# Kernel tuning notes

Hardware: AMD Instinct MI355X
Metric: run time of the kernel (lower is better)

Reference implementation:

```python
import jax, jax.numpy as jnp
import numpy as np

D_MODEL = 1024
N_HEADS = 16
D_HEAD = 64
SEQ = 2048
BATCH = 2
ATTN_SCALE = float(np.sqrt(D_HEAD))  # cfg.use_attn_scale = True
NEG_INF = -1e9


def setup_inputs() -> dict:
    key = jax.random.key(0)
    ks = jax.random.split(key, 8)
    s = 0.02
    return {
        "query_input": jax.random.normal(ks[0], (BATCH, SEQ, D_MODEL), jnp.float32),
        "key_input": jax.random.normal(ks[1], (BATCH, SEQ, D_MODEL), jnp.float32),
        "value_input": jax.random.normal(ks[2], (BATCH, SEQ, D_MODEL), jnp.float32),
        "W_Q": jax.random.normal(ks[3], (N_HEADS, D_MODEL, D_HEAD), jnp.float32) * s,
        "W_K": jax.random.normal(ks[4], (N_HEADS, D_MODEL, D_HEAD), jnp.float32) * s,
        "W_V": jax.random.normal(ks[5], (N_HEADS, D_MODEL, D_HEAD), jnp.float32) * s,
        "W_O": jax.random.normal(ks[6], (N_HEADS, D_HEAD, D_MODEL), jnp.float32) * s,
        "b_Q": jnp.zeros((N_HEADS, D_HEAD), jnp.float32),
        "b_K": jnp.zeros((N_HEADS, D_HEAD), jnp.float32),
        "b_V": jnp.zeros((N_HEADS, D_HEAD), jnp.float32),
        "b_O": jnp.zeros((D_MODEL,), jnp.float32),
    }


def reference(query_input, key_input, value_input, W_Q, W_K, W_V, W_O, b_Q, b_K, b_V, b_O):
    # QKV projections: [batch, pos, d_model] x [head, d_model, d_head] -> [batch, pos, head, d_head]
    q = jnp.einsum("bpd,hde->bphe", query_input, W_Q) + b_Q
    k = jnp.einsum("bpd,hde->bphe", key_input, W_K) + b_K
    v = jnp.einsum("bpd,hde->bphe", value_input, W_V) + b_V

    # attn scores [batch, head, query_pos, key_pos]
    scores = jnp.einsum("bqhe,bkhe->bhqk", q, k) / ATTN_SCALE

    # causal mask (attn_type == 'global'): tril over [n_ctx, n_ctx] sliced to seq
    causal = jnp.tril(jnp.ones((SEQ, SEQ), bool))
    scores = jnp.where(causal[None, None, :, :], scores, NEG_INF)

    pattern = jax.nn.softmax(scores, axis=-1)

    # z: [batch, query_pos, head, d_head]
    z = jnp.einsum("bhqk,bkhe->bqhe", pattern, v)

    # output projection: [batch, pos, d_model]
    out = jnp.einsum("bqhe,hed->bqd", z, W_O) + b_O
    return out
```

## Files before the change

### kernel.cpp

```cpp
#include <hip/hip_runtime.h>
#include <stdint.h>


typedef __attribute__((ext_vector_type(8))) short short8;
typedef __attribute__((ext_vector_type(4))) short short4v;
typedef __attribute__((ext_vector_type(4))) float floatx4;
typedef __attribute__((ext_vector_type(4))) unsigned int uintx4;
typedef __attribute__((ext_vector_type(2))) unsigned int uint2v;

#define MFMA16(a, b, c) __builtin_amdgcn_mfma_f32_16x16x32_bf16(a, b, c, 0, 0, 0)

#if __has_builtin(__builtin_amdgcn_mfma_f32_16x16x16bf16_1k)
#define HAVE_K16 1
#define MFMAK16(a, b, c) __builtin_amdgcn_mfma_f32_16x16x16bf16_1k(a, b, c, 0, 0, 0)
#else
#define HAVE_K16 0
#endif

__device__ __forceinline__ unsigned short f2b(float f) {
  unsigned int u = __builtin_bit_cast(unsigned int, f);
  u = (u + 0x7fffu + ((u >> 16) & 1u)) >> 16;
  return (unsigned short)u;
}
__device__ __forceinline__ float exp2f_fast(float x) {
#if __has_builtin(__builtin_amdgcn_exp2f)
  return __builtin_amdgcn_exp2f(x);
#else
  return exp2f(x);
#endif
}
__device__ __forceinline__ unsigned int pack2_bf16(float lo, float hi) {
#if __has_builtin(__builtin_amdgcn_perm)
  return __builtin_amdgcn_perm(__builtin_bit_cast(unsigned int, hi),
                               __builtin_bit_cast(unsigned int, lo), 0x07060302u);
#else
  return (__builtin_bit_cast(unsigned int, lo) >> 16) |
         (__builtin_bit_cast(unsigned int, hi) & 0xffff0000u);
#endif
}

__device__ __forceinline__ void async_copy16(void* lds, const void* g) {
  __builtin_amdgcn_global_load_lds(
      (const __attribute__((address_space(1))) unsigned int*)g,
      (__attribute__((address_space(3))) unsigned int*)lds, 16, 0, 0);
}

__device__ __forceinline__ void xpose4(floatx4& v, int lane) {
  {
    float s0 = __shfl_xor(v[1], 1, 64);
    float s1 = __shfl_xor(v[0], 1, 64);
    float s2 = __shfl_xor(v[3], 1, 64);
    float s3 = __shfl_xor(v[2], 1, 64);
    if (lane & 1) { v[0] = s0; v[2] = s2; } else { v[1] = s1; v[3] = s3; }
  }
  {
    float s0 = __shfl_xor(v[2], 2, 64);
    float s1 = __shfl_xor(v[3], 2, 64);
    float s2 = __shfl_xor(v[0], 2, 64);
    float s3 = __shfl_xor(v[1], 2, 64);
    if (lane & 2) { v[0] = s0; v[1] = s1; } else { v[2] = s2; v[3] = s3; }
  }
}

__global__ __launch_bounds__(256) void convall(
    const float* __restrict__ Xq, const float* __restrict__ Xk,
    const float* __restrict__ Xv, const float* __restrict__ WQ,
    const float* __restrict__ WK, const float* __restrict__ WV,
    const float* __restrict__ WO, unsigned short* __restrict__ xout,
    unsigned short* __restrict__ wout, unsigned short* __restrict__ woout) {
  __shared__ float T[64][65];
  const int bid = blockIdx.x;
  const int t = threadIdx.x;
  if (bid < 12288) {
    const int yy = bid / 4096, x = bid - yy * 4096;
    const float* in = (yy == 0) ? Xq : ((yy == 1) ? Xk : Xv);
    size_t i = (size_t)x * 256 + t;
    float4 v = ((const float4*)in)[i];
    ushort4 u;
    u.x = f2b(v.x); u.y = f2b(v.y); u.z = f2b(v.z); u.w = f2b(v.w);
    ((ushort4*)(xout + (size_t)yy * 4194304))[i] = u;
    return;
  }
  const int rr = t >> 4, cc = t & 15;
  if (bid < 13056) {
    const int sub = bid - 12288;
    const int yy = sub >> 8, x = sub & 255;
    const float* in = (yy == 0) ? WQ : ((yy == 1) ? WK : WV);
    const int h = x >> 4, d0 = (x & 15) << 6;
#pragma unroll
    for (int it = 0; it < 4; ++it) {
      int dl = it * 16 + rr;
      float4 v = *(const float4*)&in[(size_t)h * 65536 + (size_t)(d0 + dl) * 64 + cc * 4];
      T[dl][cc * 4 + 0] = v.x; T[dl][cc * 4 + 1] = v.y;
      T[dl][cc * 4 + 2] = v.z; T[dl][cc * 4 + 3] = v.w;
    }
    __syncthreads();
    unsigned short* ob = wout + (size_t)yy * 1048576;
#pragma unroll
    for (int it = 0; it < 4; ++it) {
      int e = it * 16 + rr;
      ushort4 u;
      u.x = f2b(T[cc * 4 + 0][e]); u.y = f2b(T[cc * 4 + 1][e]);
      u.z = f2b(T[cc * 4 + 2][e]); u.w = f2b(T[cc * 4 + 3][e]);
      *(ushort4*)&ob[(size_t)(h * 64 + e) * 1024 + d0 + cc * 4] = u;
    }
    return;
  }
  {
    const int x = bid - 13056;
    const int r0 = (x & 15) << 6, c0 = (x >> 4) << 6;
#pragma unroll
    for (int it = 0; it < 4; ++it) {
      int rl = it * 16 + rr;
      float4 v = *(const float4*)&WO[(size_t)(r0 + rl) * 1024 + c0 + cc * 4];
      T[rl][cc * 4 + 0] = v.x; T[rl][cc * 4 + 1] = v.y;
      T[rl][cc * 4 + 2] = v.z; T[rl][cc * 4 + 3] = v.w;
    }
    __syncthreads();
#pragma unroll
    for (int it = 0; it < 4; ++it) {
      int dl = it * 16 + rr;
      ushort4 u;
      u.x = f2b(T[cc * 4 + 0][dl]); u.y = f2b(T[cc * 4 + 1][dl]);
      u.z = f2b(T[cc * 4 + 2][dl]); u.w = f2b(T[cc * 4 + 3][dl]);
      *(ushort4*)&woout[(size_t)(c0 + dl) * 1024 + r0 + cc * 4] = u;
    }
  }
}

template <int TM, int NZ>
__global__ __launch_bounds__(512, (TM == 128) ? 6 : 4) void gemm512(
    const short* __restrict__ A0, const short* __restrict__ A1,
    const short* __restrict__ A2, const short* __restrict__ B0,
    const short* __restrict__ B1, const short* __restrict__ B2,
    const float* __restrict__ bias0, const float* __restrict__ bias1,
    const float* __restrict__ bias2, unsigned short* __restrict__ ob0,
    unsigned short* __restrict__ ob1, unsigned short* __restrict__ ob2,
    float* __restrict__ outf, float qscale) {
  constexpr int WAVES_N = (TM == 128) ? 2 : 4;
  constexpr int NJ = (TM == 128) ? 4 : 2;
  constexpr int NY = 4096 / TM;
  __shared__ short As[TM * 64];
  __shared__ short Bs[128 * 64];

  const int L = blockIdx.x;
  const int x = L / (NY * NZ);
  const int r = L - x * (NY * NZ);
  const int y = r / NZ;
  const int z = r - y * NZ;

  const short* A = (z == 0) ? A0 : (z == 1) ? A1 : A2;
  const short* Bt = (z == 0) ? B0 : (z == 1) ? B1 : B2;

  const int tid = threadIdx.x;
  const int lane = tid & 63, w = tid >> 6;
  const int quad = lane >> 4, col = lane & 15;
  const int m0 = y * TM, n0 = x * 128;
  const int wm = (w / WAVES_N) * 32, wn = (w % WAVES_N) * (NJ * 16);

  floatx4 acc[2][NJ] = {};

  const int slr = lane >> 3, sgc = (lane & 7) ^ slr;
  const short* ga = A + (size_t)(m0 + w * (TM / 8) + slr) * 1024 + sgc * 8;
  const short* gb = Bt + (size_t)(n0 + w * 16 + slr) * 1024 + sgc * 8;
  const int fsw = col & 7;

  for (int k0 = 0; k0 < 1024; k0 += 64) {
    if (TM == 128) {
      async_copy16(&As[(w * 16) * 64], ga);
      async_copy16(&As[(w * 16 + 8) * 64], ga + 8 * 1024);
    } else {
      async_copy16(&As[(w * 8) * 64], ga);
    }
    async_copy16(&Bs[(w * 16) * 64], gb);
    async_copy16(&Bs[(w * 16 + 8) * 64], gb + 8 * 1024);
    ga += 64; gb += 64;
    __syncthreads();
#pragma unroll
    for (int kk = 0; kk < 2; ++kk) {
      short8 af[2], bf[NJ];
#pragma unroll
      for (int mi = 0; mi < 2; ++mi)
        af[mi] = *(const short8*)&As[(wm + mi * 16 + col) * 64 +
                                     (((kk * 4 + quad) ^ fsw) * 8)];
#pragma unroll
      for (int nj = 0; nj < NJ; ++nj)
        bf[nj] = *(const short8*)&Bs[(wn + nj * 16 + col) * 64 +
                                     (((kk * 4 + quad) ^ fsw) * 8)];
#pragma unroll
      for (int mi = 0; mi < 2; ++mi)
#pragma unroll
        for (int nj = 0; nj < NJ; ++nj)
          acc[mi][nj] = MFMA16(af[mi], bf[nj], acc[mi][nj]);
    }
    __syncthreads();
  }

  const float* bias = (z == 0) ? bias0 : (z == 1) ? bias1 : bias2;
  unsigned short* outb = (z == 0) ? ob0 : (z == 1) ? ob1 : ob2;
  const int mode = (NZ == 3) ? ((z == 2) ? 2 : 1) : 0;
  const float scale = (NZ == 3 && z == 0) ? qscale : 1.0f;

  float bv[NJ];
#pragma unroll
  for (int nj = 0; nj < NJ; ++nj) bv[nj] = bias[n0 + wn + nj * 16 + col];

  if (mode == 2) {
#pragma unroll
    for (int mi = 0; mi < 2; ++mi)
#pragma unroll
      for (int nj = 0; nj < NJ; ++nj) {
        int m = m0 + wm + mi * 16 + quad * 4;
        int n = n0 + wn + nj * 16 + col;
        int bb = m >> 11, s = m & 2047, h = n >> 6, e = n & 63;
        ushort4 u;
        u.x = f2b(acc[mi][nj][0] + bv[nj]);
        u.y = f2b(acc[mi][nj][1] + bv[nj]);
        u.z = f2b(acc[mi][nj][2] + bv[nj]);
        u.w = f2b(acc[mi][nj][3] + bv[nj]);
        *(ushort4*)&outb[(((size_t)bb * 16 + h) * 64 + e) * 2048 + s] = u;
      }
  } else {
#pragma unroll
    for (int mi = 0; mi < 2; ++mi)
#pragma unroll
      for (int nj = 0; nj < NJ; ++nj) {
        floatx4 v;
#pragma unroll
        for (int rr = 0; rr < 4; ++rr) v[rr] = (acc[mi][nj][rr] + bv[nj]) * scale;
        xpose4(v, lane);
        int m = m0 + wm + mi * 16 + quad * 4 + (col & 3);
        int nb = n0 + wn + nj * 16 + (col & ~3);
        if (mode == 0) {
          *(floatx4*)&outf[(size_t)m * 1024 + nb] = v;
        } else {
          int bb = m >> 11, s = m & 2047, h = nb >> 6, e = nb & 63;
          ushort4 u;
          u.x = f2b(v[0]); u.y = f2b(v[1]); u.z = f2b(v[2]); u.w = f2b(v[3]);
          *(ushort4*)&outb[(((size_t)bb * 16 + h) * 2048 + s) * 64 + e] = u;
        }
      }
  }
}

#if !HAVE_K16
__device__ __forceinline__ void exchange4(const unsigned int* u01,
                                          const unsigned int* u23, int srcA,
                                          int srcB, bool hiq, short8& pf0,
                                          short8& pf1) {
  unsigned int xA0 = (unsigned int)__shfl((int)u01[0], srcA, 64);
  unsigned int xA1 = (unsigned int)__shfl((int)u01[1], srcA, 64);
  unsigned int yA0 = (unsigned int)__shfl((int)u23[0], srcA, 64);
  unsigned int yA1 = (unsigned int)__shfl((int)u23[1], srcA, 64);
  unsigned int xB0 = (unsigned int)__shfl((int)u01[0], srcB, 64);
  unsigned int xB1 = (unsigned int)__shfl((int)u01[1], srcB, 64);
  unsigned int yB0 = (unsigned int)__shfl((int)u23[0], srcB, 64);
  unsigned int yB1 = (unsigned int)__shfl((int)u23[1], srcB, 64);
  uintx4 v0;
  v0.x = hiq ? xA1 : xA0; v0.y = hiq ? yA1 : yA0;
  v0.z = hiq ? xB1 : xB0; v0.w = hiq ? yB1 : yB0;
  pf0 = __builtin_bit_cast(short8, v0);
  xA0 = (unsigned int)__shfl((int)u01[2], srcA, 64);
  xA1 = (unsigned int)__shfl((int)u01[3], srcA, 64);
  yA0 = (unsigned int)__shfl((int)u23[2], srcA, 64);
  yA1 = (unsigned int)__shfl((int)u23[3], srcA, 64);
  xB0 = (unsigned int)__shfl((int)u01[2], srcB, 64);
  xB1 = (unsigned int)__shfl((int)u01[3], srcB, 64);
  yB0 = (unsigned int)__shfl((int)u23[2], srcB, 64);
  yB1 = (unsigned int)__shfl((int)u23[3], srcB, 64);
  uintx4 v1;
  v1.x = hiq ? xA1 : xA0; v1.y = hiq ? yA1 : yA0;
  v1.z = hiq ? xB1 : xB0; v1.w = hiq ? yB1 : yB0;
  pf1 = __builtin_bit_cast(short8, v1);
}
#endif

__device__ __forceinline__ void stage_kv(short* Kbuf, short* Vbuf,
                                         const short* kg, const short* vg,
                                         int kv0, int w, int slr, int sgc) {
  const short* kr = kg + (size_t)(kv0 + w * 16 + slr) * 64 + sgc * 8;
  async_copy16(&Kbuf[(w * 16) * 64], kr);
  async_copy16(&Kbuf[(w * 16 + 8) * 64], kr + 8 * 64);
  const short* vr = vg + (size_t)(w * 16 + slr) * 2048 + kv0 + sgc * 8;
  async_copy16(&Vbuf[(w * 16) * 64], vr);
  async_copy16(&Vbuf[(w * 16 + 8) * 64], vr + 8 * 2048);
}

__global__ __launch_bounds__(256) void attn(const short* __restrict__ q,
                                            const short* __restrict__ k,
                                            const short* __restrict__ vt,
                                            unsigned short* __restrict__ z) {
  __shared__ short Ks[2][64 * 64];
  __shared__ short Vs[2][64 * 64];

  const int tid = threadIdx.x;
  const int lane = tid & 63, w = tid >> 6;
  const int quad = lane >> 4, col = lane & 15;
  const int qt = 31 - (blockIdx.x >> 5), bh = blockIdx.x & 31;
  const int q0 = qt * 64, qw0 = q0 + w * 16;
  const size_t base = (size_t)bh * (2048 * 64);

  const short* qp = q + base + (size_t)(qw0 + col) * 64 + quad * 8;
  short8 bq0 = *(const short8*)qp;
  short8 bq1 = *(const short8*)(qp + 32);

  floatx4 o[4] = {};
  float m_run = -1e30f, l_run = 0.f;

  const short* kg = k + base;
  const short* vg = vt + base;
  const int ksw = col & 7;
  const int slr = lane >> 3, sgc = (lane & 7) ^ slr;
#if !HAVE_K16
  const int srcA = ((quad & 1) << 5) + col, srcB = srcA + 16;
  const bool hiq = (quad & 2) != 0;
#endif

  stage_kv(Ks[0], Vs[0], kg, vg, 0, w, slr, sgc);
  int p = 0;

  for (int t = 0; t <= qt; ++t) {
    __syncthreads();
    if (t < qt) stage_kv(Ks[p ^ 1], Vs[p ^ 1], kg, vg, (t + 1) * 64, w, slr, sgc);

    const bool diag = (t == qt);
    const int mtmax = diag ? w : 3;

    floatx4 st[4];
#pragma unroll
    for (int mt = 0; mt < 4; ++mt) {
      if (mt <= mtmax) {
        const short* kb = &Ks[p][(mt * 16 + col) * 64];
        short8 ka0 = *(const short8*)(kb + (quad ^ ksw) * 8);
        short8 ka1 = *(const short8*)(kb + ((quad + 4) ^ ksw) * 8);
        floatx4 a = {0.f, 0.f, 0.f, 0.f};
        a = MFMA16(ka0, bq0, a);
        a = MFMA16(ka1, bq1, a);
        if (diag && mt == mtmax) {
#pragma unroll
          for (int r = 0; r < 4; ++r)
            if (quad * 4 + r > col) a[r] = -1e9f;
        }
        st[mt] = a;
      }
    }

    float pmax = -3e38f;
#pragma unroll
    for (int mt = 0; mt < 4; ++mt)
      if (mt <= mtmax) {
#pragma unroll
        for (int r = 0; r < 4; ++r) pmax = fmaxf(pmax, st[mt][r]);
      }
    pmax = fmaxf(pmax, __shfl_xor(pmax, 16, 64));
    pmax = fmaxf(pmax, __shfl_xor(pmax, 32, 64));
    float mnew = fmaxf(m_run, pmax);
    float alpha = exp2f_fast(m_run - mnew);
    m_run = mnew;

    unsigned int u01[4], u23[4];
    float lsum = 0.f;
#pragma unroll
    for (int mt = 0; mt < 4; ++mt) {
      if (mt <= mtmax) {
        float p0 = exp2f_fast(st[mt][0] - mnew);
        float p1 = exp2f_fast(st[mt][1] - mnew);
        float p2 = exp2f_fast(st[mt][2] - mnew);
        float p3 = exp2f_fast(st[mt][3] - mnew);
        lsum += (p0 + p1) + (p2 + p3);
        u01[mt] = pack2_bf16(p0, p1);
        u23[mt] = pack2_bf16(p2, p3);
      } else {
        u01[mt] = 0u; u23[mt] = 0u;
      }
    }
    lsum += __shfl_xor(lsum, 16, 64);
    lsum += __shfl_xor(lsum, 32, 64);
    l_run = l_run * alpha + lsum;

#if HAVE_K16
    short4v pb[4];
#pragma unroll
    for (int mt = 0; mt < 4; ++mt) {
      uint2v uu;
      uu.x = u01[mt]; uu.y = u23[mt];
      pb[mt] = __builtin_bit_cast(short4v, uu);
    }
#pragma unroll
    for (int et = 0; et < 4; ++et) {
      const short* vrow = &Vs[p][(et * 16 + col) * 64];
      floatx4 t0 = o[et];
#pragma unroll
      for (int r = 0; r < 4; ++r) t0[r] *= alpha;
#pragma unroll
      for (int mt = 0; mt < 4; ++mt) {
        if (mt <= mtmax) {
          int c = mt * 2 + (quad >> 1);
          short4v va = *(const short4v*)&vrow[((c ^ ksw) * 8) + (quad & 1) * 4];
          t0 = MFMAK16(va, pb[mt], t0);
        }
      }
      o[et] = t0;
    }
#else
    short8 pf0, pf1;
    exchange4(u01, u23, srcA, srcB, hiq, pf0, pf1);
#pragma unroll
    for (int et = 0; et < 4; ++et) {
      const short* vb = &Vs[p][(et * 16 + col) * 64];
      short8 va0 = *(const short8*)(vb + (quad ^ ksw) * 8);
      short8 va1 = *(const short8*)(vb + ((quad + 4) ^ ksw) * 8);
      floatx4 t0 = o[et];
#pragma unroll
      for (int r = 0; r < 4; ++r) t0[r] *= alpha;
      t0 = MFMA16(va0, pf0, t0);
      t0 = MFMA16(va1, pf1, t0);
      o[et] = t0;
    }
#endif
    p ^= 1;
  }

  const int b = bh >> 4, h = bh & 15;
#if __has_builtin(__builtin_amdgcn_rcpf)
  const float invl = __builtin_amdgcn_rcpf(l_run);
#else
  const float invl = 1.f / l_run;
#endif
  unsigned short* zr = z + (((size_t)b * 2048 + qw0 + col) * 16 + h) * 64;
#pragma unroll
  for (int et = 0; et < 4; ++et) {
    ushort4 u;
    u.x = f2b(o[et][0] * invl); u.y = f2b(o[et][1] * invl);
    u.z = f2b(o[et][2] * invl); u.w = f2b(o[et][3] * invl);
    *(ushort4*)&zr[et * 16 + quad * 4] = u;
  }
}

extern "C" void kernel_launch(void* const* d_in, const int* in_sizes, int n_in,
                              void* d_out, int out_size, void* d_ws, size_t ws_size,
                              hipStream_t stream) {
  (void)in_sizes; (void)n_in; (void)out_size; (void)ws_size;
  const float* Xq = (const float*)d_in[0];
  const float* Xk = (const float*)d_in[1];
  const float* Xv = (const float*)d_in[2];
  const float* WQ = (const float*)d_in[3];
  const float* WK = (const float*)d_in[4];
  const float* WV = (const float*)d_in[5];
  const float* WO = (const float*)d_in[6];
  const float* bQ = (const float*)d_in[7];
  const float* bK = (const float*)d_in[8];
  const float* bV = (const float*)d_in[9];
  const float* bO = (const float*)d_in[10];
  float* out = (float*)d_out;

  unsigned short* xqb = (unsigned short*)d_ws;
  unsigned short* xkb = xqb + 4194304;
  unsigned short* xvb = xkb + 4194304;
  unsigned short* wqt = xvb + 4194304;
  unsigned short* wkt = wqt + 1048576;
  unsigned short* wvt = wkt + 1048576;
  unsigned short* wot = wvt + 1048576;
  unsigned short* qb = wot + 1048576;
  unsigned short* kb = qb + 4194304;
  unsigned short* vtb = kb + 4194304;
  unsigned short* zb = vtb + 4194304;

  convall<<<13312, 256, 0, stream>>>(Xq, Xk, Xv, WQ, WK, WV, WO, xqb, wqt, wot);

  const float qscale = 0.125f * 1.44269504088896f;
  gemm512<128, 3><<<768, 512, 0, stream>>>(
      (const short*)xqb, (const short*)xkb, (const short*)xvb,
      (const short*)wqt, (const short*)wkt, (const short*)wvt, bQ, bK, bV, qb,
      kb, vtb, nullptr, qscale);

  attn<<<1024, 256, 0, stream>>>((const short*)qb, (const short*)kb,
                                 (const short*)vtb, zb);

  gemm512<64, 1><<<512, 512, 0, stream>>>(
      (const short*)zb, (const short*)zb, (const short*)zb, (const short*)wot,
      (const short*)wot, (const short*)wot, bO, bO, bO, nullptr, nullptr,
      nullptr, out, 1.0f);
}
```

Measured before the change: 218.4 us.

## Split-K the output projection GEMM with atomic accumulation

Splits the K dimension of the output-projection GEMM into two halves, which doubles the block count from 512 to 1024 to fill the GPU better. Each half adds its partial sum into the float output with atomicAdd, and only the first half adds the bias. The output now has to be zeroed by a memset first. That adds an extra pass over 16 MB of memory plus scalar atomic traffic, and the launch bounds for the TM=64 variant change as well.

Result: slower. 312.3 us (+43.0%).

```diff
diff --git a/kernel.cpp b/kernel.cpp
--- a/kernel.cpp
+++ b/kernel.cpp
@@ -128,8 +128,8 @@
   }
 }
 
-template <int TM, int NZ>
-__global__ __launch_bounds__(512, (TM == 128) ? 6 : 4) void gemm512(
+template <int TM, int NZ, int KS>
+__global__ __launch_bounds__(512, 6) void gemm512(
     const short* __restrict__ A0, const short* __restrict__ A1,
     const short* __restrict__ A2, const short* __restrict__ B0,
     const short* __restrict__ B1, const short* __restrict__ B2,
@@ -144,10 +144,12 @@
   __shared__ short Bs[128 * 64];
 
   const int L = blockIdx.x;
-  const int x = L / (NY * NZ);
-  const int r = L - x * (NY * NZ);
-  const int y = r / NZ;
-  const int z = r - y * NZ;
+  const int x = L / (NY * NZ * KS);
+  const int r0d = L - x * (NY * NZ * KS);
+  const int y = r0d / (NZ * KS);
+  const int r1d = r0d - y * (NZ * KS);
+  const int z = r1d / KS;
+  const int ks = r1d - z * KS;
 
   const short* A = (z == 0) ? A0 : (z == 1) ? A1 : A2;
   const short* Bt = (z == 0) ? B0 : (z == 1) ? B1 : B2;
@@ -161,11 +163,12 @@
   floatx4 acc[2][NJ] = {};
 
   const int slr = lane >> 3, sgc = (lane & 7) ^ slr;
-  const short* ga = A + (size_t)(m0 + w * (TM / 8) + slr) * 1024 + sgc * 8;
-  const short* gb = Bt + (size_t)(n0 + w * 16 + slr) * 1024 + sgc * 8;
+  const int kbase = ks * (1024 / KS);
+  const short* ga = A + (size_t)(m0 + w * (TM / 8) + slr) * 1024 + kbase + sgc * 8;
+  const short* gb = Bt + (size_t)(n0 + w * 16 + slr) * 1024 + kbase + sgc * 8;
   const int fsw = col & 7;
 
-  for (int k0 = 0; k0 < 1024; k0 += 64) {
+  for (int k0 = 0; k0 < 1024 / KS; k0 += 64) {
     if (TM == 128) {
       async_copy16(&As[(w * 16) * 64], ga);
       async_copy16(&As[(w * 16 + 8) * 64], ga + 8 * 1024);
@@ -200,6 +203,7 @@
   unsigned short* outb = (z == 0) ? ob0 : (z == 1) ? ob1 : ob2;
   const int mode = (NZ == 3) ? ((z == 2) ? 2 : 1) : 0;
   const float scale = (NZ == 3 && z == 0) ? qscale : 1.0f;
+  const float bmul = (KS == 1 || ks == 0) ? 1.0f : 0.0f;
 
   float bv[NJ];
 #pragma unroll
@@ -227,12 +231,21 @@
       for (int nj = 0; nj < NJ; ++nj) {
         floatx4 v;
 #pragma unroll
-        for (int rr = 0; rr < 4; ++rr) v[rr] = (acc[mi][nj][rr] + bv[nj]) * scale;
+        for (int rr = 0; rr < 4; ++rr)
+          v[rr] = (acc[mi][nj][rr] + bv[nj] * bmul) * scale;
         xpose4(v, lane);
         int m = m0 + wm + mi * 16 + quad * 4 + (col & 3);
         int nb = n0 + wn + nj * 16 + (col & ~3);
         if (mode == 0) {
-          *(floatx4*)&outf[(size_t)m * 1024 + nb] = v;
+          float* op = &outf[(size_t)m * 1024 + nb];
+          if (KS == 2) {
+            atomicAdd(op + 0, v[0]);
+            atomicAdd(op + 1, v[1]);
+            atomicAdd(op + 2, v[2]);
+            atomicAdd(op + 3, v[3]);
+          } else {
+            *(floatx4*)op = v;
+          }
         } else {
           int bb = m >> 11, s = m & 2047, h = nb >> 6, e = nb & 63;
           ushort4 u;
@@ -466,10 +479,12 @@
   unsigned short* vtb = kb + 4194304;
   unsigned short* zb = vtb + 4194304;
 
+  hipMemsetAsync(out, 0, (size_t)4096 * 1024 * sizeof(float), stream);
+
   convall<<<13312, 256, 0, stream>>>(Xq, Xk, Xv, WQ, WK, WV, WO, xqb, wqt, wot);
 
   const float qscale = 0.125f * 1.44269504088896f;
-  gemm512<128, 3><<<768, 512, 0, stream>>>(
+  gemm512<128, 3, 1><<<768, 512, 0, stream>>>(
       (const short*)xqb, (const short*)xkb, (const short*)xvb,
       (const short*)wqt, (const short*)wkt, (const short*)wvt, bQ, bK, bV, qb,
       kb, vtb, nullptr, qscale);
@@ -477,7 +492,7 @@
   attn<<<1024, 256, 0, stream>>>((const short*)qb, (const short*)kb,
                                  (const short*)vtb, zb);
 
-  gemm512<64, 1><<<512, 512, 0, stream>>>(
+  gemm512<64, 1, 2><<<1024, 512, 0, stream>>>(
       (const short*)zb, (const short*)zb, (const short*)zb, (const short*)wot,
       (const short*)wot, (const short*)wot, bO, bO, bO, nullptr, nullptr,
       nullptr, out, 1.0f);
```
